# Kernel tuning notes

Hardware: AMD Instinct MI355X
Metric: run time of the kernel (lower is better)

## Reference

```python
import jax, jax.numpy as jnp
import numpy as np

B, S, D, H, HD, E, DE = 2, 512, 768, 12, 64, 50, 50  # batch, seq, input_dim, heads, head_dim, edge_dim, dep_embed_dim


def setup_inputs() -> dict:
    key = jax.random.key(0)
    ks = jax.random.split(key, 16)
    def xn(k, shape, s=0.02):
        return (jax.random.normal(k, shape, jnp.float32) * s)
    return {
        'weight_prob_softmax': jax.random.uniform(ks[0], (B, S, S, E), jnp.float32),
        'weight_adj': jax.random.normal(ks[1], (B, S, S, E), jnp.float32),
        'gcn_inputs': jax.random.normal(ks[2], (B, S, D), jnp.float32),
        'self_loop': jax.random.uniform(ks[3], (B, S, S, E), jnp.float32),
        # self.linear
        'W_lin': xn(ks[4], (D, D)), 'b_lin': jnp.zeros((D,), jnp.float32),
        # additive attention vectors fc_w1 / fc_w2 (stored [H, HD])
        'fc_w1': xn(ks[5], (H, HD), 0.2), 'fc_w2': xn(ks[6], (H, HD), 0.2),
        # edge_mlp: Linear(E,128) -> ReLU -> (Dropout eval) -> Linear(128,H)
        'We1': xn(ks[7], (128, E), 0.1), 'be1': jnp.zeros((128,), jnp.float32),
        'We2': xn(ks[8], (H, 128), 0.1), 'be2': jnp.zeros((H,), jnp.float32),
        # self.W output projection
        'W_out': xn(ks[9], (D, D)), 'b_out': jnp.zeros((D,), jnp.float32),
        # LayerNorm params
        'ln_a': jnp.ones((D,), jnp.float32), 'ln_b': jnp.zeros((D,), jnp.float32),
        # highway.W split into column blocks: [edge | edge_i | edge_j | node1 | node2]
        'Wh_e': xn(ks[10], (DE, E), 0.1), 'Wh_ei': xn(ks[11], (DE, E), 0.1),
        'Wh_ej': xn(ks[12], (DE, E), 0.1), 'Wh_n1': xn(ks[13], (DE, D), 0.05),
        'Wh_n2': xn(ks[14], (DE, D), 0.05), 'bh': jnp.zeros((DE,), jnp.float32),
    }


def reference(weight_prob_softmax, weight_adj, gcn_inputs, self_loop,
              W_lin, b_lin, fc_w1, fc_w2, We1, be1, We2, be2,
              W_out, b_out, ln_a, ln_b, Wh_e, Wh_ei, Wh_ej, Wh_n1, Wh_n2, bh):
    wps = self_loop + weight_prob_softmax                      # [B,S,S,E]
    mask = jnp.sum(wps, axis=-1) == 0.0                        # [B,S,S]
    feature = (gcn_inputs @ W_lin.T + b_lin).reshape(B, S, H, HD)
    attn_src = jnp.einsum('bshd,hd->bhs', feature, fc_w1)      # [B,H,S]
    attn_dst = jnp.einsum('bshd,hd->bhs', feature, fc_w2)      # [B,H,S]
    # edge MLP bias (dropout is identity in eval)
    hmid = jax.nn.relu(jnp.einsum('bije,fe->bijf', wps, We1) + be1)  # [B,S,S,128]
    A = jnp.einsum('bijf,hf->bhij', hmid, We2) + be2[None, :, None, None]  # [B,H,S,S]
    attn = jax.nn.leaky_relu(attn_src[:, :, :, None] + attn_dst[:, :, None, :] + A,
                             negative_slope=0.01)
    attn = jnp.where(mask[:, None, :, :], -jnp.inf, attn)
    attn = jax.nn.softmax(attn, axis=-1)
    gcn = jnp.einsum('bhij,bjhd->bihd', attn, feature).reshape(B, S, D)
    gcn = gcn @ W_out.T + b_out
    # torch LayerNorm variant: unbiased std, divide by (std + eps)
    mean = jnp.mean(gcn, axis=-1, keepdims=True)
    std = jnp.std(gcn, axis=-1, ddof=1, keepdims=True)
    gcn = ln_a * (gcn - mean) / (std + 1e-6) + ln_b
    node = jax.nn.relu(gcn)                                    # [B,S,D]
    # RefiningStrategy: W([edge, edge_i, edge_j, node1, node2]) via block matmuls
    ediag = jnp.diagonal(weight_adj, axis1=1, axis2=2).transpose(0, 2, 1)  # [B,S,E]
    edge_out = (jnp.einsum('bije,fe->bijf', weight_adj, Wh_e)
                + (ediag @ Wh_ei.T)[:, :, None, :]             # edge_i[b,i,j]=diag[b,i]
                + (ediag @ Wh_ej.T)[:, None, :, :]             # edge_j[b,i,j]=diag[b,j]
                + (node @ Wh_n1.T)[:, None, :, :]              # node1[b,i,j]=node[b,j]
                + (node @ Wh_n2.T)[:, :, None, :]              # node2[b,i,j]=node[b,i]
                + bh)                                          # [B,S,S,DE]
    return node, edge_out
```

## Files before the change

### kernel.cpp

```cpp
#include <hip/hip_runtime.h>
#include <math.h>
#include <stddef.h>

#define BB 2
#define SS 512
#define DD 768
#define HH 12
#define HDIM 64
#define EE 50
#define DE 50
#define F1 128

typedef float f32x4 __attribute__((ext_vector_type(4)));
typedef short s16x8 __attribute__((ext_vector_type(8)));

static __device__ __forceinline__ unsigned short f2bf(float x) {
  unsigned int u = __float_as_uint(x);
  unsigned int r = u + 0x7fffu + ((u >> 16) & 1u);
  return (unsigned short)(r >> 16);
}
static __device__ __forceinline__ float bf2f(unsigned short b) {
  return __uint_as_float(((unsigned int)b) << 16);
}

__global__ __launch_bounds__(256) void k_gemm_bias(
    const float* __restrict__ X, int ldx,
    const float* __restrict__ W,
    const float* __restrict__ bias,
    float* __restrict__ Y, int ldy,
    int M, int N, int K)
{
  __shared__ float Xs[32][68];
  __shared__ float Ws[32][68];
  int t = threadIdx.x;
  int tx = t & 15, ty = t >> 4;
  int m0 = blockIdx.y * 64, n0 = blockIdx.x * 64;
  float acc[4][4] = {};
  for (int k0 = 0; k0 < K; k0 += 32) {
#pragma unroll
    for (int q = 0; q < 2; ++q) {
      int idx = t + q * 256;
      int r = idx >> 3, c = (idx & 7) << 2;
      float4 v = *(const float4*)(X + (size_t)(m0 + r) * ldx + k0 + c);
      Xs[c + 0][r] = v.x; Xs[c + 1][r] = v.y; Xs[c + 2][r] = v.z; Xs[c + 3][r] = v.w;
      float4 w = *(const float4*)(W + (size_t)(n0 + r) * K + k0 + c);
      Ws[c + 0][r] = w.x; Ws[c + 1][r] = w.y; Ws[c + 2][r] = w.z; Ws[c + 3][r] = w.w;
    }
    __syncthreads();
#pragma unroll
    for (int kk = 0; kk < 32; ++kk) {
      float a[4], b[4];
#pragma unroll
      for (int u = 0; u < 4; ++u) a[u] = Xs[kk][ty * 4 + u];
#pragma unroll
      for (int u = 0; u < 4; ++u) b[u] = Ws[kk][tx * 4 + u];
#pragma unroll
      for (int i = 0; i < 4; ++i)
#pragma unroll
        for (int j = 0; j < 4; ++j) acc[i][j] += a[i] * b[j];
    }
    __syncthreads();
  }
#pragma unroll
  for (int i = 0; i < 4; ++i) {
    int m = m0 + ty * 4 + i;
#pragma unroll
    for (int j = 0; j < 4; ++j) {
      int n = n0 + tx * 4 + j;
      Y[(size_t)m * ldy + n] = acc[i][j] + bias[n];
    }
  }
}

__global__ __launch_bounds__(192) void k_attnvec(
    const float* __restrict__ feat, const float* __restrict__ w1,
    const float* __restrict__ w2, float* __restrict__ src, float* __restrict__ dst)
{
  int bs = blockIdx.x;
  int t = threadIdx.x;
  int h = t >> 4, l = t & 15;
  float4 f = *(const float4*)(feat + (size_t)bs * DD + h * HDIM + l * 4);
  float4 a = *(const float4*)(w1 + h * HDIM + l * 4);
  float4 c = *(const float4*)(w2 + h * HDIM + l * 4);
  float ps = f.x * a.x + f.y * a.y + f.z * a.z + f.w * a.w;
  float pd = f.x * c.x + f.y * c.y + f.z * c.z + f.w * c.w;
#pragma unroll
  for (int o = 8; o > 0; o >>= 1) {
    ps += __shfl_xor(ps, o);
    pd += __shfl_xor(pd, o);
  }
  if (l == 0) {
    int b = bs >> 9, s = bs & 511;
    src[((b * HH + h) << 9) + s] = ps;
    dst[((b * HH + h) << 9) + s] = pd;
  }
}

__global__ __launch_bounds__(64) void k_prep(
    const float* __restrict__ We1, const float* __restrict__ be1,
    const float* __restrict__ We2, const float* __restrict__ Whe,
    s16x8* __restrict__ wtab, float* __restrict__ betab,
    s16x8* __restrict__ wtabE)
{
  const int l = threadIdx.x;
  const int lr = l & 15, lg = l >> 4;
#pragma unroll
  for (int ks = 0; ks < 2; ++ks)
#pragma unroll
    for (int n = 0; n < 8; ++n) {
      s16x8 v;
#pragma unroll
      for (int u = 0; u < 8; ++u) {
        int e = ks * 32 + lg * 8 + u;
        float x = (e < 50) ? We1[(n * 16 + lr) * 50 + e] : 0.0f;
        v[u] = (short)f2bf(x);
      }
      wtab[(ks * 8 + n) * 64 + l] = v;
    }
#pragma unroll
  for (int kk = 0; kk < 4; ++kk) {
    s16x8 v;
#pragma unroll
    for (int u = 0; u < 8; ++u) {
      int f = kk * 32 + lg * 8 + u;
      v[u] = (short)((lr < 12) ? f2bf(We2[lr * 128 + f]) : (unsigned short)0);
    }
    wtab[(16 + kk) * 64 + l] = v;
  }
#pragma unroll
  for (int n = 0; n < 8; ++n) betab[n * 64 + l] = be1[n * 16 + lr];
#pragma unroll
  for (int nt = 0; nt < 4; ++nt)
#pragma unroll
    for (int ks = 0; ks < 2; ++ks) {
      int f = nt * 16 + lr;
      s16x8 v;
#pragma unroll
      for (int u = 0; u < 8; ++u) {
        int e = ks * 32 + lg * 8 + u;
        float x = (f < 50 && e < 50) ? Whe[f * 50 + e] : 0.0f;
        v[u] = (short)f2bf(x);
      }
      wtabE[(nt * 2 + ks) * 64 + l] = v;
    }
}

__global__ __launch_bounds__(256, 4) void k_scores_mfma(
    const float* __restrict__ wprob, const float* __restrict__ sloop,
    const s16x8* __restrict__ wtab, const float* __restrict__ betab,
    const float* __restrict__ be2,
    const float* __restrict__ src, const float* __restrict__ dst,
    float* __restrict__ scores)
{
  __shared__ unsigned short hmid_s[128][72];
  __shared__ float masks[128];

  const int blk = blockIdx.x;
  const int c = blk & 3;
  const int i = (blk >> 2) & 511;
  const int b = blk >> 11;
  const int j0c = c << 7;
  const int t = threadIdx.x;
  const int w = t >> 6, l = t & 63;
  const int lr = l & 15, lg = l >> 4;
  const int jbase = w * 32;

  int offs[8];
  bool vmask[8];
#pragma unroll
  for (int s8 = 0; s8 < 8; ++s8) {
    int ks = s8 >> 2, q = s8 & 3;
    int off = ks * 32 + lg * 8 + 2 * q;
    vmask[s8] = (off <= 48);
    offs[s8] = vmask[s8] ? off : 0;
  }
  const size_t rowbase = ((size_t)(b * SS + i) * SS + j0c) * EE;
  float2 pA[2][8], pS[2][8];
#pragma unroll
  for (int jt = 0; jt < 2; ++jt) {
    const int jl = jbase + jt * 16 + lr;
    const float* wrow = wprob + rowbase + (size_t)jl * EE;
    const float* srow = sloop + rowbase + (size_t)jl * EE;
#pragma unroll
    for (int s8 = 0; s8 < 8; ++s8) {
      pA[jt][s8] = *(const float2*)(wrow + offs[s8]);
      pS[jt][s8] = *(const float2*)(srow + offs[s8]);
    }
  }
  const int hc = (lr < 12) ? lr : 0;
  const float* drow = dst + ((size_t)(b * HH + hc) << 9);
  float4 dv0 = *(const float4*)(drow + j0c + jbase + lg * 4);
  float4 dv1 = *(const float4*)(drow + j0c + jbase + 16 + lg * 4);
  s16x8 wb[4];
#pragma unroll
  for (int kk = 0; kk < 4; ++kk) wb[kk] = wtab[(16 + kk) * 64 + l];
  float be1v[8];
#pragma unroll
  for (int n = 0; n < 8; ++n) be1v[n] = betab[n * 64 + l];
  const float be2v = be2[hc];
  const float srcv = src[((b * HH + hc) << 9) + i];
  __builtin_amdgcn_sched_barrier(0);

  s16x8 aA[2][2];
  float rsum[2];
#pragma unroll
  for (int jt = 0; jt < 2; ++jt) {
    float rs = 0.0f;
#pragma unroll
    for (int ks = 0; ks < 2; ++ks) {
      s16x8 f;
#pragma unroll
      for (int q = 0; q < 4; ++q) {
        int s8 = ks * 4 + q;
        float vx = vmask[s8] ? (pA[jt][s8].x + pS[jt][s8].x) : 0.0f;
        float vy = vmask[s8] ? (pA[jt][s8].y + pS[jt][s8].y) : 0.0f;
        f[2 * q] = (short)f2bf(vx);
        f[2 * q + 1] = (short)f2bf(vy);
        rs += vx + vy;
      }
      aA[jt][ks] = f;
    }
    rsum[jt] = rs;
  }
#pragma unroll
  for (int jt = 0; jt < 2; ++jt) {
    rsum[jt] += __shfl_xor(rsum[jt], 16);
    rsum[jt] += __shfl_xor(rsum[jt], 32);
  }
  if (lg == 0) {
    masks[jbase + lr] = (rsum[0] == 0.0f) ? 1.0f : 0.0f;
    masks[jbase + 16 + lr] = (rsum[1] == 0.0f) ? 1.0f : 0.0f;
  }

  f32x4 accB[2] = {};
#pragma unroll
  for (int h = 0; h < 2; ++h) {
    s16x8 wah[2][4];
#pragma unroll
    for (int ks = 0; ks < 2; ++ks)
#pragma unroll
      for (int nn = 0; nn < 4; ++nn)
        wah[ks][nn] = wtab[(ks * 8 + h * 4 + nn) * 64 + l];

    f32x4 accA[2][4] = {};
#pragma unroll
    for (int ks = 0; ks < 2; ++ks)
#pragma unroll
      for (int nn = 0; nn < 4; ++nn) {
        accA[0][nn] = __builtin_amdgcn_mfma_f32_16x16x32_bf16(aA[0][ks], wah[ks][nn], accA[0][nn], 0, 0, 0);
        accA[1][nn] = __builtin_amdgcn_mfma_f32_16x16x32_bf16(aA[1][ks], wah[ks][nn], accA[1][nn], 0, 0, 0);
      }
#pragma unroll
    for (int jt = 0; jt < 2; ++jt)
#pragma unroll
      for (int nn = 0; nn < 4; ++nn)
#pragma unroll
        for (int r = 0; r < 4; ++r) {
          float v = fmaxf(accA[jt][nn][r] + be1v[h * 4 + nn], 0.0f);
          hmid_s[jbase + jt * 16 + lg * 4 + r][nn * 16 + lr] = f2bf(v);
        }

#pragma unroll
    for (int kh = 0; kh < 2; ++kh) {
      int kk = 2 * h + kh;
      s16x8 a0 = *(const s16x8*)&hmid_s[jbase + lr][kh * 32 + lg * 8];
      s16x8 a1 = *(const s16x8*)&hmid_s[jbase + 16 + lr][kh * 32 + lg * 8];
      accB[0] = __builtin_amdgcn_mfma_f32_16x16x32_bf16(a0, wb[kk], accB[0], 0, 0, 0);
      accB[1] = __builtin_amdgcn_mfma_f32_16x16x32_bf16(a1, wb[kk], accB[1], 0, 0, 0);
    }
  }

  if (lr < 12) {
#pragma unroll
    for (int jt = 0; jt < 2; ++jt) {
      int jl = jbase + jt * 16 + lg * 4;
      const float4 dv = jt ? dv1 : dv0;
      float4 st;
#pragma unroll
      for (int r = 0; r < 4; ++r) {
        float x = accB[jt][r] + be2v + srcv + (&dv.x)[r];
        x = (x > 0.0f) ? x : 0.01f * x;
        if (masks[jl + r] != 0.0f) x = -INFINITY;
        (&st.x)[r] = x;
      }
      *(float4*)(scores + ((((size_t)(b * SS + i)) * HH + lr) << 9) + j0c + jl) = st;
    }
  }
}

__global__ __launch_bounds__(256) void k_softmax_pv(
    const float* __restrict__ scores, const float* __restrict__ feat,
    float* __restrict__ gout)
{
  __shared__ float p[2][12][512];
  int blk = blockIdx.x;
  int b = blk >> 8;
  int i0 = (blk & 255) << 1;
  int t = threadIdx.x;
  size_t base = ((size_t)(b * SS + i0) * HH) << 9;
  for (int q = t; q < 12288; q += 256) ((float*)p)[q] = scores[base + q];
  __syncthreads();

  int w = t >> 6, l = t & 63;
  for (int r = w; r < 24; r += 4) {
    int ii = r / 12, h = r % 12;
    float* row = p[ii][h];
    float vv[8];
    float m = -INFINITY;
#pragma unroll
    for (int u = 0; u < 8; ++u) {
      vv[u] = row[l + (u << 6)];
      m = fmaxf(m, vv[u]);
    }
#pragma unroll
    for (int o = 32; o > 0; o >>= 1) m = fmaxf(m, __shfl_xor(m, o));
    float s = 0.0f;
#pragma unroll
    for (int u = 0; u < 8; ++u) {
      float e = __expf(vv[u] - m);
      vv[u] = e;
      s += e;
    }
#pragma unroll
    for (int o = 32; o > 0; o >>= 1) s += __shfl_xor(s, o);
    float inv = 1.0f / s;
#pragma unroll
    for (int u = 0; u < 8; ++u) row[l + (u << 6)] = vv[u] * inv;
  }
  __syncthreads();

  float acc[2][3] = {};
  const float* fb = feat + (size_t)b * SS * DD;
  int h0 = t >> 6;
#pragma unroll 4
  for (int j = 0; j < 512; ++j) {
    const float* fr = fb + (size_t)j * DD;
    float f0 = fr[t], f1 = fr[t + 256], f2 = fr[t + 512];
    float p00 = p[0][h0][j], p10 = p[1][h0][j];
    float p01 = p[0][h0 + 4][j], p11 = p[1][h0 + 4][j];
    float p02 = p[0][h0 + 8][j], p12 = p[1][h0 + 8][j];
    acc[0][0] += p00 * f0; acc[0][1] += p01 * f1; acc[0][2] += p02 * f2;
    acc[1][0] += p10 * f0; acc[1][1] += p11 * f1; acc[1][2] += p12 * f2;
  }
#pragma unroll
  for (int ii = 0; ii < 2; ++ii)
#pragma unroll
    for (int u = 0; u < 3; ++u)
      gout[(size_t)(b * SS + i0 + ii) * DD + t + (u << 8)] = acc[ii][u];
}

__global__ __launch_bounds__(256) void k_ln(
    const float* __restrict__ gcn2, const float* __restrict__ ga,
    const float* __restrict__ gb, float* __restrict__ out)
{
  __shared__ float rs[4], rss[4];
  int row = blockIdx.x;
  int t = threadIdx.x;
  const float* x = gcn2 + (size_t)row * DD;
  float v[3];
  float s = 0.0f, ss2 = 0.0f;
#pragma unroll
  for (int u = 0; u < 3; ++u) {
    v[u] = x[t + (u << 8)];
    s += v[u];
    ss2 += v[u] * v[u];
  }
#pragma unroll
  for (int o = 32; o > 0; o >>= 1) {
    s += __shfl_down(s, o);
    ss2 += __shfl_down(ss2, o);
  }
  int w = t >> 6, l = t & 63;
  if (l == 0) { rs[w] = s; rss[w] = ss2; }
  __syncthreads();
  float S = rs[0] + rs[1] + rs[2] + rs[3];
  float SSum = rss[0] + rss[1] + rss[2] + rss[3];
  float mean = S * (1.0f / 768.0f);
  float var = (SSum - 768.0f * mean * mean) * (1.0f / 767.0f);
  var = fmaxf(var, 0.0f);
  float rinv = 1.0f / (sqrtf(var) + 1e-6f);
#pragma unroll
  for (int u = 0; u < 3; ++u) {
    int cidx = t + (u << 8);
    float y = ga[cidx] * (v[u] - mean) * rinv + gb[cidx];
    out[(size_t)row * DD + cidx] = fmaxf(y, 0.0f);
  }
}

__global__ __launch_bounds__(256) void k_pq(
    const float* __restrict__ node, const float* __restrict__ wadj,
    const float* __restrict__ Whei, const float* __restrict__ Whej,
    const float* __restrict__ Whn1, const float* __restrict__ Whn2,
    const float* __restrict__ bh, float* __restrict__ P, float* __restrict__ Q)
{
  __shared__ float nd[2][768];
  __shared__ float ed[2][64];
  const int bs0 = blockIdx.x * 2;
  const int t = threadIdx.x;
  const int w = t >> 6, l = t & 63;

  for (int q = t; q < 384; q += 256) {
    int rr = q / 192, idx = q % 192;
    *(float4*)(nd[rr] + idx * 4) =
        *(const float4*)(node + (size_t)(bs0 + rr) * DD + idx * 4);
  }
  {
    int rr = t >> 7, tt = t & 127;
    if (tt < 50) {
      int bs = bs0 + rr;
      int b = bs >> 9, s = bs & 511;
      ed[rr][tt] = wadj[((size_t)(b * SS + s) * SS + s) * EE + tt];
    }
  }
  __syncthreads();

  float4 n00 = *(const float4*)(nd[0] + l * 4);
  float4 n01 = *(const float4*)(nd[0] + 256 + l * 4);
  float4 n02 = *(const float4*)(nd[0] + 512 + l * 4);
  float4 n10 = *(const float4*)(nd[1] + l * 4);
  float4 n11 = *(const float4*)(nd[1] + 256 + l * 4);
  float4 n12 = *(const float4*)(nd[1] + 512 + l * 4);
  float el0 = (l < 50) ? ed[0][l] : 0.0f;
  float el1 = (l < 50) ? ed[1][l] : 0.0f;

  for (int o = w; o < 100; o += 4) {
    const int which = (o >= 50);
    const int f = o - which * 50;
    const float* Wn = which ? Whn1 : Whn2;
    const float* We = which ? Whej : Whei;
    const float* wr = Wn + f * DD;
    float4 w0 = *(const float4*)(wr + l * 4);
    float4 w1 = *(const float4*)(wr + 256 + l * 4);
    float4 w2 = *(const float4*)(wr + 512 + l * 4);
    float wev = (l < 50) ? We[f * EE + l] : 0.0f;
    float a0 = n00.x * w0.x + n00.y * w0.y + n00.z * w0.z + n00.w * w0.w
             + n01.x * w1.x + n01.y * w1.y + n01.z * w1.z + n01.w * w1.w
             + n02.x * w2.x + n02.y * w2.y + n02.z * w2.z + n02.w * w2.w
             + el0 * wev;
    float a1 = n10.x * w0.x + n10.y * w0.y + n10.z * w0.z + n10.w * w0.w
             + n11.x * w1.x + n11.y * w1.y + n11.z * w1.z + n11.w * w1.w
             + n12.x * w2.x + n12.y * w2.y + n12.z * w2.z + n12.w * w2.w
             + el1 * wev;
#pragma unroll
    for (int ofs = 32; ofs > 0; ofs >>= 1) {
      a0 += __shfl_xor(a0, ofs);
      a1 += __shfl_xor(a1, ofs);
    }
    if (l == 0) {
      float bias = which ? bh[f] : 0.0f;
      float* dst0 = (which ? Q : P) + (size_t)bs0 * DE + f;
      dst0[0] = a0 + bias;
      dst0[DE] = a1 + bias;
    }
  }
}

__global__ __launch_bounds__(256, 6) void k_edge_mfma(
    const float* __restrict__ wadj, const s16x8* __restrict__ wtabE,
    const float* __restrict__ P, const float* __restrict__ Q,
    float* __restrict__ eout)
{
  __shared__ __align__(16) unsigned char raw[25600];
  unsigned short (*adj_s)[72] = (unsigned short(*)[72])raw;
  float* park = (float*)raw;
  __shared__ float P_s[64];

  const int t = threadIdx.x;
  const size_t n0 = (size_t)blockIdx.x * 128;
  const int b = (int)(n0 >> 18);
  const int i = (int)((n0 & 262143) >> 9);
  const int j0 = (int)(n0 & 511);
  const int w = t >> 6, l = t & 63;
  const int lr = l & 15, lg = l >> 4;
  const int mbase = w * 32;

  float4 pw[7];
  {
    const float* wp = wadj + n0 * EE;
#pragma unroll
    for (int k = 0; k < 7; ++k)
      if (k < 6 || t < 64) pw[k] = *(const float4*)(wp + 4 * (t + 256 * k));
  }

  s16x8 we[4][2];
#pragma unroll
  for (int nt = 0; nt < 4; ++nt)
#pragma unroll
    for (int ks = 0; ks < 2; ++ks) we[nt][ks] = wtabE[(nt * 2 + ks) * 64 + l];
  if (t < 64) P_s[t] = (t < 50) ? P[(size_t)(b * SS + i) * DE + t] : 0.0f;

  for (int q = t; q < 896; q += 256) {
    int r = q / 7, cd = 25 + q % 7;
    ((unsigned int*)adj_s)[r * 36 + cd] = 0u;
  }

#pragma unroll
  for (int k = 0; k < 7; ++k)
    if (k < 6 || t < 64) {
      int f = 4 * (t + 256 * k);
      int j = f / 50;
      int e0 = f - j * 50;
#pragma unroll
      for (int u = 0; u < 4; ++u) {
        int e = e0 + u, jj = j;
        if (e >= 50) { e -= 50; jj += 1; }
        adj_s[jj][e] = f2bf((&pw[k].x)[u]);
      }
    }
  __syncthreads();

  f32x4 acc[2][4] = {};
#pragma unroll
  for (int ks = 0; ks < 2; ++ks) {
    s16x8 a0 = *(const s16x8*)&adj_s[mbase + lr][ks * 32 + lg * 8];
    s16x8 a1 = *(const s16x8*)&adj_s[mbase + 16 + lr][ks * 32 + lg * 8];
#pragma unroll
    for (int nt = 0; nt < 4; ++nt) {
      acc[0][nt] = __builtin_amdgcn_mfma_f32_16x16x32_bf16(a0, we[nt][ks], acc[0][nt], 0, 0, 0);
      acc[1][nt] = __builtin_amdgcn_mfma_f32_16x16x32_bf16(a1, we[nt][ks], acc[1][nt], 0, 0, 0);
    }
  }
  __syncthreads();

#pragma unroll
  for (int nt = 0; nt < 4; ++nt) {
    int f = nt * 16 + lr;
    if (f < 50) {
      float pf = P_s[f];
#pragma unroll
      for (int mt = 0; mt < 2; ++mt) {
        int m = mbase + mt * 16 + lg * 4;
        const float* qp = Q + (size_t)(b * SS + j0 + m) * DE + f;
#pragma unroll
        for (int r = 0; r < 4; ++r)
          park[(m + r) * DE + f] = acc[mt][nt][r] + pf + qp[r * DE];
      }
    }
  }
  __syncthreads();

  const float4* s4 = (const float4*)park;
  float4* d4 = (float4*)(eout + n0 * DE);
  for (int q = t; q < 1600; q += 256) d4[q] = s4[q];
}

extern "C" void kernel_launch(void* const* d_in, const int* in_sizes, int n_in,
                              void* d_out, int out_size, void* d_ws, size_t ws_size,
                              hipStream_t stream)
{
  const float* wprob = (const float*)d_in[0];
  const float* wadj  = (const float*)d_in[1];
  const float* gin   = (const float*)d_in[2];
  const float* sloop = (const float*)d_in[3];
  const float* W_lin = (const float*)d_in[4];
  const float* b_lin = (const float*)d_in[5];
  const float* fw1   = (const float*)d_in[6];
  const float* fw2   = (const float*)d_in[7];
  const float* We1   = (const float*)d_in[8];
  const float* be1   = (const float*)d_in[9];
  const float* We2   = (const float*)d_in[10];
  const float* be2   = (const float*)d_in[11];
  const float* W_out = (const float*)d_in[12];
  const float* b_out = (const float*)d_in[13];
  const float* ln_a  = (const float*)d_in[14];
  const float* ln_b  = (const float*)d_in[15];
  const float* Whe   = (const float*)d_in[16];
  const float* Whei  = (const float*)d_in[17];
  const float* Whej  = (const float*)d_in[18];
  const float* Whn1  = (const float*)d_in[19];
  const float* Whn2  = (const float*)d_in[20];
  const float* bh    = (const float*)d_in[21];

  float* ws = (float*)d_ws;
  float* feature = ws + 0;
  float* src     = ws + 786432;
  float* dst     = ws + 798720;
  float* scores  = ws + 811008;
  float* gcnmid  = ws + 7102464;
  float* gcn2    = ws + 7888896;
  float* P       = ws + 8675328;
  float* Q       = ws + 8726528;
  s16x8* wtab    = (s16x8*)(ws + 8777728);
  float* betab   = ws + 8782848;
  s16x8* wtabE   = (s16x8*)(ws + 8783360);

  float* node = (float*)d_out;
  float* eout = (float*)d_out + 786432;

  k_prep<<<1, 64, 0, stream>>>(We1, be1, We2, Whe, wtab, betab, wtabE);
  k_gemm_bias<<<dim3(DD / 64, (BB * SS) / 64), 256, 0, stream>>>(
      gin, DD, W_lin, b_lin, feature, DD, BB * SS, DD, DD);
  k_attnvec<<<BB * SS, 192, 0, stream>>>(feature, fw1, fw2, src, dst);
  k_scores_mfma<<<BB * SS * 4, 256, 0, stream>>>(
      wprob, sloop, wtab, betab, be2, src, dst, scores);
  k_softmax_pv<<<BB * SS / 2, 256, 0, stream>>>(scores, feature, gcnmid);
  k_gemm_bias<<<dim3(DD / 64, (BB * SS) / 64), 256, 0, stream>>>(
      gcnmid, DD, W_out, b_out, gcn2, DD, BB * SS, DD, DD);
  k_ln<<<BB * SS, 256, 0, stream>>>(gcn2, ln_a, ln_b, node);
  k_pq<<<BB * SS / 2, 256, 0, stream>>>(node, wadj, Whei, Whej, Whn1, Whn2, bh, P, Q);
  k_edge_mfma<<<(BB * SS * SS) / 128, 256, 0, stream>>>(wadj, wtabE, P, Q, eout);
}
```

Baseline: 315.1 us.

## Fuse edge-MLP score computation into softmax-PV kernel to skip scores buffer

The per-edge attention score kernel and the softmax/PV kernel are merged into one. Each block now loops over its two query rows and four column chunks, writing scores straight into the shared-memory tile that softmax reads. This removes the global write and read-back of the full [B,S,H,S] scores tensor and one kernel launch. In exchange the grid drops from 4096 blocks to 512, each doing eight serial iterations, and occupancy is lowered to two blocks per CU. That reduces the parallelism available to hide latency on the large wprob and self_loop streams.

```diff
diff --git a/kernel.cpp b/kernel.cpp
--- a/kernel.cpp
+++ b/kernel.cpp
@@ -145,25 +145,36 @@
     }
 }
 
-__global__ __launch_bounds__(256, 4) void k_scores_mfma(
+__global__ __launch_bounds__(256, 2) void k_fused_attn(
     const float* __restrict__ wprob, const float* __restrict__ sloop,
     const s16x8* __restrict__ wtab, const float* __restrict__ betab,
     const float* __restrict__ be2,
     const float* __restrict__ src, const float* __restrict__ dst,
-    float* __restrict__ scores)
-{
+    const float* __restrict__ feat, float* __restrict__ gout)
+{
+  __shared__ float p[2][12][512];
   __shared__ unsigned short hmid_s[128][72];
   __shared__ float masks[128];
 
   const int blk = blockIdx.x;
-  const int c = blk & 3;
-  const int i = (blk >> 2) & 511;
-  const int b = blk >> 11;
-  const int j0c = c << 7;
+  const int b = blk >> 8;
+  const int i0 = (blk & 255) << 1;
   const int t = threadIdx.x;
   const int w = t >> 6, l = t & 63;
   const int lr = l & 15, lg = l >> 4;
   const int jbase = w * 32;
+
+  s16x8 wb[4];
+#pragma unroll
+  for (int kk = 0; kk < 4; ++kk) wb[kk] = wtab[(16 + kk) * 64 + l];
+  float be1v[8];
+#pragma unroll
+  for (int n = 0; n < 8; ++n) be1v[n] = betab[n * 64 + l];
+  const int hc = (lr < 12) ? lr : 0;
+  const float be2v = be2[hc];
+  const float srcv_[2] = {src[((b * HH + hc) << 9) + i0],
+                          src[((b * HH + hc) << 9) + i0 + 1]};
+  const float* drow = dst + ((size_t)(b * HH + hc) << 9);
 
   int offs[8];
   bool vmask[8];
@@ -174,134 +185,117 @@
     vmask[s8] = (off <= 48);
     offs[s8] = vmask[s8] ? off : 0;
   }
-  const size_t rowbase = ((size_t)(b * SS + i) * SS + j0c) * EE;
-  float2 pA[2][8], pS[2][8];
-#pragma unroll
-  for (int jt = 0; jt < 2; ++jt) {
-    const int jl = jbase + jt * 16 + lr;
-    const float* wrow = wprob + rowbase + (size_t)jl * EE;
-    const float* srow = sloop + rowbase + (size_t)jl * EE;
-#pragma unroll
-    for (int s8 = 0; s8 < 8; ++s8) {
-      pA[jt][s8] = *(const float2*)(wrow + offs[s8]);
-      pS[jt][s8] = *(const float2*)(srow + offs[s8]);
-    }
-  }
-  const int hc = (lr < 12) ? lr : 0;
-  const float* drow = dst + ((size_t)(b * HH + hc) << 9);
-  float4 dv0 = *(const float4*)(drow + j0c + jbase + lg * 4);
-  float4 dv1 = *(const float4*)(drow + j0c + jbase + 16 + lg * 4);
-  s16x8 wb[4];
-#pragma unroll
-  for (int kk = 0; kk < 4; ++kk) wb[kk] = wtab[(16 + kk) * 64 + l];
-  float be1v[8];
-#pragma unroll
-  for (int n = 0; n < 8; ++n) be1v[n] = betab[n * 64 + l];
-  const float be2v = be2[hc];
-  const float srcv = src[((b * HH + hc) << 9) + i];
-  __builtin_amdgcn_sched_barrier(0);
-
-  s16x8 aA[2][2];
-  float rsum[2];
-#pragma unroll
-  for (int jt = 0; jt < 2; ++jt) {
-    float rs = 0.0f;
-#pragma unroll
-    for (int ks = 0; ks < 2; ++ks) {
-      s16x8 f;
-#pragma unroll
-      for (int q = 0; q < 4; ++q) {
-        int s8 = ks * 4 + q;
-        float vx = vmask[s8] ? (pA[jt][s8].x + pS[jt][s8].x) : 0.0f;
-        float vy = vmask[s8] ? (pA[jt][s8].y + pS[jt][s8].y) : 0.0f;
-        f[2 * q] = (short)f2bf(vx);
-        f[2 * q + 1] = (short)f2bf(vy);
-        rs += vx + vy;
-      }
-      aA[jt][ks] = f;
-    }
-    rsum[jt] = rs;
-  }
-#pragma unroll
-  for (int jt = 0; jt < 2; ++jt) {
-    rsum[jt] += __shfl_xor(rsum[jt], 16);
-    rsum[jt] += __shfl_xor(rsum[jt], 32);
-  }
-  if (lg == 0) {
-    masks[jbase + lr] = (rsum[0] == 0.0f) ? 1.0f : 0.0f;
-    masks[jbase + 16 + lr] = (rsum[1] == 0.0f) ? 1.0f : 0.0f;
-  }
-
-  f32x4 accB[2] = {};
-#pragma unroll
-  for (int h = 0; h < 2; ++h) {
-    s16x8 wah[2][4];
-#pragma unroll
-    for (int ks = 0; ks < 2; ++ks)
-#pragma unroll
-      for (int nn = 0; nn < 4; ++nn)
-        wah[ks][nn] = wtab[(ks * 8 + h * 4 + nn) * 64 + l];
-
-    f32x4 accA[2][4] = {};
-#pragma unroll
-    for (int ks = 0; ks < 2; ++ks)
-#pragma unroll
-      for (int nn = 0; nn < 4; ++nn) {
-        accA[0][nn] = __builtin_amdgcn_mfma_f32_16x16x32_bf16(aA[0][ks], wah[ks][nn], accA[0][nn], 0, 0, 0);
-        accA[1][nn] = __builtin_amdgcn_mfma_f32_16x16x32_bf16(aA[1][ks], wah[ks][nn], accA[1][nn], 0, 0, 0);
-      }
-#pragma unroll
-    for (int jt = 0; jt < 2; ++jt)
-#pragma unroll
-      for (int nn = 0; nn < 4; ++nn)
+
+#pragma unroll 2
+  for (int it = 0; it < 8; ++it) {
+    const int ii = it >> 2, c = it & 3;
+    const int i = i0 + ii;
+    const int j0c = c << 7;
+
+    const size_t rowbase = ((size_t)(b * SS + i) * SS + j0c) * EE;
+    float2 pA[2][8], pS[2][8];
+#pragma unroll
+    for (int jt = 0; jt < 2; ++jt) {
+      const int jl = jbase + jt * 16 + lr;
+      const float* wrow = wprob + rowbase + (size_t)jl * EE;
+      const float* srow = sloop + rowbase + (size_t)jl * EE;
+#pragma unroll
+      for (int s8 = 0; s8 < 8; ++s8) {
+        pA[jt][s8] = *(const float2*)(wrow + offs[s8]);
+        pS[jt][s8] = *(const float2*)(srow + offs[s8]);
+      }
+    }
+    float4 dv0 = *(const float4*)(drow + j0c + jbase + lg * 4);
+    float4 dv1 = *(const float4*)(drow + j0c + jbase + 16 + lg * 4);
+
+    s16x8 aA[2][2];
+    float rsum[2];
+#pragma unroll
+    for (int jt = 0; jt < 2; ++jt) {
+      float rs = 0.0f;
+#pragma unroll
+      for (int ks = 0; ks < 2; ++ks) {
+        s16x8 f;
+#pragma unroll
+        for (int q = 0; q < 4; ++q) {
+          int s8 = ks * 4 + q;
+          float vx = vmask[s8] ? (pA[jt][s8].x + pS[jt][s8].x) : 0.0f;
+          float vy = vmask[s8] ? (pA[jt][s8].y + pS[jt][s8].y) : 0.0f;
+          f[2 * q] = (short)f2bf(vx);
+          f[2 * q + 1] = (short)f2bf(vy);
+          rs += vx + vy;
+        }
+        aA[jt][ks] = f;
+      }
+      rsum[jt] = rs;
+    }
+#pragma unroll
+    for (int jt = 0; jt < 2; ++jt) {
+      rsum[jt] += __shfl_xor(rsum[jt], 16);
+      rsum[jt] += __shfl_xor(rsum[jt], 32);
+    }
+    if (lg == 0) {
+      masks[jbase + lr] = (rsum[0] == 0.0f) ? 1.0f : 0.0f;
+      masks[jbase + 16 + lr] = (rsum[1] == 0.0f) ? 1.0f : 0.0f;
+    }
+
+    f32x4 accB[2] = {};
+#pragma unroll
+    for (int h = 0; h < 2; ++h) {
+      s16x8 wah[2][4];
+#pragma unroll
+      for (int ks = 0; ks < 2; ++ks)
+#pragma unroll
+        for (int nn = 0; nn < 4; ++nn)
+          wah[ks][nn] = wtab[(ks * 8 + h * 4 + nn) * 64 + l];
+
+      f32x4 accA[2][4] = {};
+#pragma unroll
+      for (int ks = 0; ks < 2; ++ks)
+#pragma unroll
+        for (int nn = 0; nn < 4; ++nn) {
+          accA[0][nn] = __builtin_amdgcn_mfma_f32_16x16x32_bf16(aA[0][ks], wah[ks][nn], accA[0][nn], 0, 0, 0);
+          accA[1][nn] = __builtin_amdgcn_mfma_f32_16x16x32_bf16(aA[1][ks], wah[ks][nn], accA[1][nn], 0, 0, 0);
+        }
+#pragma unroll
+      for (int jt = 0; jt < 2; ++jt)
+#pragma unroll
+        for (int nn = 0; nn < 4; ++nn)
+#pragma unroll
+          for (int r = 0; r < 4; ++r) {
+            float v = fmaxf(accA[jt][nn][r] + be1v[h * 4 + nn], 0.0f);
+            hmid_s[jbase + jt * 16 + lg * 4 + r][nn * 16 + lr] = f2bf(v);
+          }
+#pragma unroll
+      for (int kh = 0; kh < 2; ++kh) {
+        int kk = 2 * h + kh;
+        s16x8 a0 = *(const s16x8*)&hmid_s[jbase + lr][kh * 32 + lg * 8];
+        s16x8 a1 = *(const s16x8*)&hmid_s[jbase + 16 + lr][kh * 32 + lg * 8];
+        accB[0] = __builtin_amdgcn_mfma_f32_16x16x32_bf16(a0, wb[kk], accB[0], 0, 0, 0);
+        accB[1] = __builtin_amdgcn_mfma_f32_16x16x32_bf16(a1, wb[kk], accB[1], 0, 0, 0);
+      }
+    }
+
+    if (lr < 12) {
+      const float srcv = srcv_[ii];
+#pragma unroll
+      for (int jt = 0; jt < 2; ++jt) {
+        int jl = jbase + jt * 16 + lg * 4;
+        const float4 dv = jt ? dv1 : dv0;
+        float4 st;
 #pragma unroll
         for (int r = 0; r < 4; ++r) {
-          float v = fmaxf(accA[jt][nn][r] + be1v[h * 4 + nn], 0.0f);
-          hmid_s[jbase + jt * 16 + lg * 4 + r][nn * 16 + lr] = f2bf(v);
+          float x = accB[jt][r] + be2v + srcv + (&dv.x)[r];
+          x = (x > 0.0f) ? x : 0.01f * x;
+          if (masks[jl + r] != 0.0f) x = -INFINITY;
+          (&st.x)[r] = x;
         }
-
-#pragma unroll
-    for (int kh = 0; kh < 2; ++kh) {
-      int kk = 2 * h + kh;
-      s16x8 a0 = *(const s16x8*)&hmid_s[jbase + lr][kh * 32 + lg * 8];
-      s16x8 a1 = *(const s16x8*)&hmid_s[jbase + 16 + lr][kh * 32 + lg * 8];
-      accB[0] = __builtin_amdgcn_mfma_f32_16x16x32_bf16(a0, wb[kk], accB[0], 0, 0, 0);
-      accB[1] = __builtin_amdgcn_mfma_f32_16x16x32_bf16(a1, wb[kk], accB[1], 0, 0, 0);
-    }
-  }
-
-  if (lr < 12) {
-#pragma unroll
-    for (int jt = 0; jt < 2; ++jt) {
-      int jl = jbase + jt * 16 + lg * 4;
-      const float4 dv = jt ? dv1 : dv0;
-      float4 st;
-#pragma unroll
-      for (int r = 0; r < 4; ++r) {
-        float x = accB[jt][r] + be2v + srcv + (&dv.x)[r];
-        x = (x > 0.0f) ? x : 0.01f * x;
-        if (masks[jl + r] != 0.0f) x = -INFINITY;
-        (&st.x)[r] = x;
-      }
-      *(float4*)(scores + ((((size_t)(b * SS + i)) * HH + lr) << 9) + j0c + jl) = st;
-    }
-  }
-}
-
-__global__ __launch_bounds__(256) void k_softmax_pv(
-    const float* __restrict__ scores, const float* __restrict__ feat,
-    float* __restrict__ gout)
-{
-  __shared__ float p[2][12][512];
-  int blk = blockIdx.x;
-  int b = blk >> 8;
-  int i0 = (blk & 255) << 1;
-  int t = threadIdx.x;
-  size_t base = ((size_t)(b * SS + i0) * HH) << 9;
-  for (int q = t; q < 12288; q += 256) ((float*)p)[q] = scores[base + q];
-  __syncthreads();
-
-  int w = t >> 6, l = t & 63;
+        *(float4*)&p[ii][lr][j0c + jl] = st;
+      }
+    }
+  }
+  __syncthreads();
+
   for (int r = w; r < 24; r += 4) {
     int ii = r / 12, h = r % 12;
     float* row = p[ii][h];
@@ -575,7 +569,6 @@
   float* feature = ws + 0;
   float* src     = ws + 786432;
   float* dst     = ws + 798720;
-  float* scores  = ws + 811008;
   float* gcnmid  = ws + 7102464;
   float* gcn2    = ws + 7888896;
   float* P       = ws + 8675328;
@@ -591,9 +584,8 @@
   k_gemm_bias<<<dim3(DD / 64, (BB * SS) / 64), 256, 0, stream>>>(
       gin, DD, W_lin, b_lin, feature, DD, BB * SS, DD, DD);
   k_attnvec<<<BB * SS, 192, 0, stream>>>(feature, fw1, fw2, src, dst);
-  k_scores_mfma<<<BB * SS * 4, 256, 0, stream>>>(
-      wprob, sloop, wtab, betab, be2, src, dst, scores);
-  k_softmax_pv<<<BB * SS / 2, 256, 0, stream>>>(scores, feature, gcnmid);
+  k_fused_attn<<<BB * SS / 2, 256, 0, stream>>>(
+      wprob, sloop, wtab, betab, be2, src, dst, feature, gcnmid);
   k_gemm_bias<<<dim3(DD / 64, (BB * SS) / 64), 256, 0, stream>>>(
       gcnmid, DD, W_out, b_out, gcn2, DD, BB * SS, DD, DD);
   k_ln<<<BB * SS, 256, 0, stream>>>(gcn2, ln_a, ln_b, node);
```

New measurement: 301.9 us. 1.04x faster.
